# Optimization experiments

Hardware: AMD Instinct MI355X
Metric: run time of the kernel (lower is better)

## Reference

```python
import jax, jax.numpy as jnp
import numpy as np

TAU = 1.0
TOP_P = 0.9
EPS = 1e-5


def _nucleus_adj(X, W1, W2, W3):
    h = jnp.tanh(X @ W1.T)            # [N, d_attn]
    q = h @ W2.T                      # [N, d_attn]
    k = X @ W3.T                      # [N, d_attn]
    scores = (q @ k.T) / TAU          # [N, N]
    probs = jax.nn.softmax(scores, axis=-1)
    # nucleus (top-p): keep smallest prefix of desc-sorted probs covering mass p
    order = jnp.argsort(-probs, axis=-1)
    sp = jnp.take_along_axis(probs, order, axis=-1)
    cs = jnp.cumsum(sp, axis=-1)
    keep_sorted = (cs - sp) < TOP_P   # keep tokens before mass exceeds p (incl. crossing one)
    inv = jnp.argsort(order, axis=-1)
    keep = jnp.take_along_axis(keep_sorted, inv, axis=-1)
    A = jnp.where(keep, probs, 0.0)
    return A / jnp.sum(A, axis=-1, keepdims=True)


def _sequence_priors(N, dtype):
    # forward/backward chain priors (S=None case): row-stochastic shift matrices
    Rf = jnp.eye(N, k=-1, dtype=dtype).at[0, 0].set(1.0)
    Rb = jnp.eye(N, k=1, dtype=dtype).at[N - 1, N - 1].set(1.0)
    return Rf, Rb


def setup_inputs() -> dict:
    key = jax.random.key(0)
    ks = jax.random.split(key, 8)
    N, d_in, d_attn, steps = 4096, 512, 64, 2
    s = 0.02
    return {
        "X": jax.random.normal(ks[0], (N, d_in), jnp.float32),
        "W1": jax.random.normal(ks[1], (d_attn, d_in), jnp.float32) * s,
        "W2": jax.random.normal(ks[2], (d_attn, d_attn), jnp.float32) * s,
        "W3": jax.random.normal(ks[3], (d_attn, d_in), jnp.float32) * s,
        "U1": jax.random.normal(ks[4], (steps, d_in, d_in), jnp.float32) * s,
        "U2": jax.random.normal(ks[5], (steps, d_in, d_in), jnp.float32) * s,
        "U3": jax.random.normal(ks[6], (steps, d_in, d_in), jnp.float32) * s,
        "gamma": jnp.ones((d_in,), jnp.float32),
        "beta": jnp.zeros((d_in,), jnp.float32),
    }


def reference(X, W1, W2, W3, U1, U2, U3, gamma, beta):
    N = X.shape[0]
    steps = U1.shape[0]
    Rf, Rb = _sequence_priors(N, X.dtype)
    Z = jnp.zeros_like(X)
    Xf, Xb, Xa = X, X, X
    for n in range(steps):
        A = _nucleus_adj(Xa, W1, W2, W3)
        Xf = Rf @ Xf
        Xb = Rb @ Xb
        Xa = A @ Xa
        P = Xf @ U1[n].T + Xb @ U2[n].T
        F = Xa @ U3[n].T
        Z = Z + (P + F)  # dropout is identity in eval mode
    y = X + Z
    mu = jnp.mean(y, axis=-1, keepdims=True)
    var = jnp.var(y, axis=-1, keepdims=True)
    return (y - mu) * jax.lax.rsqrt(var + EPS) * gamma + beta
```

## Files before the change

kernel.cpp:

```cpp
#include <hip/hip_runtime.h>
#include <hip/hip_bf16.h>
#include <math.h>

typedef short bf16x8 __attribute__((ext_vector_type(8)));
typedef float f32x4 __attribute__((ext_vector_type(4)));
typedef unsigned short u16;

#define N_TOK  4096
#define D_IN   512
#define D_ATTN 64
#define NBI    1024
#define CAPW   128
#define TOPP   0.9f
#define LN_EPS 1e-5f
#define AMAXV  (N_TOK - 1)
#define FLTMAX 3.402823466e38f
#define MSCALE 524288.0f

__device__ __forceinline__ u16 f2bf(float f) {
  unsigned int u = __float_as_uint(f);
  return (u16)((u + 0x7FFFu + ((u >> 16) & 1u)) >> 16);
}

__device__ __forceinline__ unsigned mfix(float e) {
  return (unsigned)(e * MSCALE + 0.5f);
}

__device__ __forceinline__ void gload16(const u16* g, u16* l) {
  __builtin_amdgcn_global_load_lds(
      (const __attribute__((address_space(1))) unsigned int*)g,
      (__attribute__((address_space(3))) unsigned int*)l, 16, 0, 0);
}

template<int EPI, int NSEG, int KSEG, int BN>
__global__ __launch_bounds__(256)
void gemm128(const u16* __restrict__ A0, int lda0, int sh0, const u16* __restrict__ B0, int ldb0,
             const u16* __restrict__ A1, int lda1, int sh1, const u16* __restrict__ B1, int ldb1,
             const u16* __restrict__ A2, int lda2, int sh2, const u16* __restrict__ B2, int ldb2,
             float* __restrict__ Cf, u16* __restrict__ Cb, u16* __restrict__ CbT,
             int ldc, int ldct)
{
  constexpr int NF = BN / 32;
  __shared__ u16 sA[2][128 * 64];
  __shared__ u16 sB[2][BN * 64];

  const int tid  = threadIdx.x;
  const int wave = tid >> 6;
  const int lane = tid & 63;
  const int l15  = lane & 15;
  const int l4   = lane >> 4;
  const int brow = blockIdx.y << 7;
  const int bcol = blockIdx.x * BN;
  const int kz   = blockIdx.z * KSEG;
  const int wr64 = (wave >> 1) << 6;
  const int wcol = (wave & 1) * (BN >> 1);

  constexpr int IPSEG = KSEG >> 6;
  constexpr int TOTAL = NSEG * IPSEG;

  auto stage = [&](int buf, int it) {
    int seg = (NSEG == 1) ? 0 : (it / IPSEG);
    int kk  = (NSEG == 1) ? (it << 6) : ((it % IPSEG) << 6);
    const u16 *Ab, *Bb; int la, lb, sh;
    if (seg == 0)      { Ab = A0; la = lda0; sh = sh0; Bb = B0; lb = ldb0; }
    else if (seg == 1) { Ab = A1; la = lda1; sh = sh1; Bb = B1; lb = ldb1; }
    else               { Ab = A2; la = lda2; sh = sh2; Bb = B2; lb = ldb2; }
    kk += kz;
#pragma unroll
    for (int q = 0; q < 4; ++q) {
      int idx = q * 256 + tid;
      int row = idx >> 3;
      int chunk = (idx & 7) ^ (row & 7);
      int r = brow + row + sh;
      r = (r < 0) ? 0 : ((r > AMAXV) ? AMAXV : r);
      gload16(Ab + (size_t)r * la + kk + chunk * 8, &sA[buf][idx * 8]);
    }
#pragma unroll
    for (int q = 0; q < BN / 32; ++q) {
      int idx = q * 256 + tid;
      int row = idx >> 3;
      int chunk = (idx & 7) ^ (row & 7);
      gload16(Bb + (size_t)(bcol + row) * lb + kk + chunk * 8, &sB[buf][idx * 8]);
    }
  };

  f32x4 acc[4][NF];
#pragma unroll
  for (int m = 0; m < 4; ++m)
#pragma unroll
    for (int n = 0; n < NF; ++n) {
      acc[m][n][0] = 0.f; acc[m][n][1] = 0.f; acc[m][n][2] = 0.f; acc[m][n][3] = 0.f;
    }

  stage(0, 0);
  asm volatile("s_waitcnt vmcnt(0)" ::: "memory");
  __builtin_amdgcn_s_barrier();

  for (int i = 0; i < TOTAL; ++i) {
    const int c = i & 1;
    if (i + 1 < TOTAL) stage(c ^ 1, i + 1);
#pragma unroll
    for (int ks = 0; ks < 2; ++ks) {
      bf16x8 af[4], bfr[NF];
#pragma unroll
      for (int m = 0; m < 4; ++m) {
        int ar = wr64 + m * 16 + l15;
        af[m] = *(const bf16x8*)&sA[c][ar * 64 + (((ks << 2) + l4) ^ (ar & 7)) * 8];
      }
#pragma unroll
      for (int n = 0; n < NF; ++n) {
        int br = wcol + n * 16 + l15;
        bfr[n] = *(const bf16x8*)&sB[c][br * 64 + (((ks << 2) + l4) ^ (br & 7)) * 8];
      }
#pragma unroll
      for (int m = 0; m < 4; ++m)
#pragma unroll
        for (int n = 0; n < NF; ++n)
          acc[m][n] = __builtin_amdgcn_mfma_f32_16x16x32_bf16(af[m], bfr[n], acc[m][n], 0, 0, 0);
    }
    asm volatile("s_waitcnt vmcnt(0)" ::: "memory");
    __builtin_amdgcn_s_barrier();
  }

  float* Cf6 = (EPI == 6 && blockIdx.z) ? (float*)CbT : Cf;
#pragma unroll
  for (int m = 0; m < 4; ++m)
#pragma unroll
    for (int n = 0; n < NF; ++n)
#pragma unroll
      for (int r = 0; r < 4; ++r) {
        const int row = brow + wr64 + m * 16 + l4 * 4 + r;
        const int col = bcol + wcol + n * 16 + l15;
        const float v = acc[m][n][r];
        if (EPI == 0) Cf[(size_t)row * ldc + col] = v;
        if (EPI == 1) Cb[(size_t)row * ldc + col] = f2bf(tanhf(v));
        if (EPI == 2) Cb[(size_t)row * ldc + col] = f2bf(v);
        if (EPI == 3) Cf[(size_t)row * ldc + col] += v;
        if (EPI == 4) {
          u16 hv = f2bf(v);
          Cb [(size_t)row * ldc  + col] = hv;
          CbT[(size_t)col * ldct + row] = hv;
        }
        if (EPI == 5) {
          if (col < 64) Cb [(size_t)row * 64 + col]        = f2bf(tanhf(v));
          else          CbT[(size_t)row * 64 + (col - 64)] = f2bf(v);
        }
        if (EPI == 6) Cf6[(size_t)row * ldc + col] = v;
      }
}

__global__ __launch_bounds__(256)
void pvfix(const float* __restrict__ Zp0, const float* __restrict__ Zp1,
           u16* __restrict__ Xa, u16* __restrict__ XaT)
{
  __shared__ u16 tile[64][65];
  const int bx = blockIdx.x, by = blockIdx.y;
  const int t = threadIdx.x;
  const int tx = t & 15, ty = t >> 4;
#pragma unroll
  for (int i = 0; i < 4; ++i) {
    int r = by * 64 + ty + 16 * i;
    int c = bx * 64 + tx * 4;
    float4 a = *(const float4*)&Zp0[(size_t)r * D_IN + c];
    float4 b = *(const float4*)&Zp1[(size_t)r * D_IN + c];
    u16 q0 = f2bf(a.x + b.x), q1 = f2bf(a.y + b.y);
    u16 q2 = f2bf(a.z + b.z), q3 = f2bf(a.w + b.w);
    *(ushort4*)&Xa[(size_t)r * D_IN + c] = make_ushort4(q0, q1, q2, q3);
    tile[ty + 16 * i][tx * 4 + 0] = q0;
    tile[ty + 16 * i][tx * 4 + 1] = q1;
    tile[ty + 16 * i][tx * 4 + 2] = q2;
    tile[ty + 16 * i][tx * 4 + 3] = q3;
  }
  __syncthreads();
#pragma unroll
  for (int i = 0; i < 4; ++i) {
    int cc = ty + 16 * i;
    int rq = tx * 4;
    u16 o0 = tile[rq + 0][cc], o1 = tile[rq + 1][cc];
    u16 o2 = tile[rq + 2][cc], o3 = tile[rq + 3][cc];
    *(ushort4*)&XaT[(size_t)(bx * 64 + cc) * N_TOK + by * 64 + rq] =
        make_ushort4(o0, o1, o2, o3);
  }
}

__global__ __launch_bounds__(256)
void nucleus_block(const float* __restrict__ S, u16* __restrict__ A, int apitch)
{
  const int t = threadIdx.x;
  const int wv = t >> 6, ln = t & 63;

  __shared__ unsigned hist[4][NBI];
  __shared__ float ge[CAPW];
  __shared__ int   gcol[CAPW];
  __shared__ unsigned gm[CAPW];
  __shared__ unsigned char kf[CAPW];
  __shared__ float sMin[4], sMax[4], sDen[4];
  __shared__ int   sCnt[4], sS[4];
  __shared__ unsigned sScan[4];
  __shared__ unsigned s_Ab;
  __shared__ int   s_cnt;

  for (int rr = 0; rr < 2; ++rr) {
    const int row = blockIdx.x + rr * (N_TOK / 2);
    const float* srow = S + (size_t)row * N_TOK;
    u16* arow = A + (size_t)row * apitch;

    __syncthreads();

    float evf[16];
    float lmax = -FLTMAX, lmin = FLTMAX;
#pragma unroll
    for (int q = 0; q < 4; ++q) {
      float4 v = ((const float4*)srow)[q * 256 + t];
      evf[4*q+0] = v.x; evf[4*q+1] = v.y; evf[4*q+2] = v.z; evf[4*q+3] = v.w;
      lmax = fmaxf(lmax, fmaxf(fmaxf(v.x, v.y), fmaxf(v.z, v.w)));
      lmin = fminf(lmin, fminf(fminf(v.x, v.y), fminf(v.z, v.w)));
    }
#pragma unroll
    for (int o = 32; o; o >>= 1) {
      lmax = fmaxf(lmax, __shfl_xor(lmax, o));
      lmin = fminf(lmin, __shfl_xor(lmin, o));
    }
    if (ln == 0) { sMax[wv] = lmax; sMin[wv] = lmin; }
    __syncthreads();
    const float smax = fmaxf(fmaxf(sMax[0], sMax[1]), fmaxf(sMax[2], sMax[3]));
    const float smin = fminf(fminf(sMin[0], sMin[1]), fminf(sMin[2], sMin[3]));

#pragma unroll
    for (int j = 0; j < 16; ++j) evf[j] = __expf(evf[j] - smax);

    unsigned keepM = 0, cand = 0xFFFFu;
    unsigned Agt = 0, T = 0;
    bool haveT = false;
    float lo = __expf(smin - smax);
    float width = fmaxf(1.0f - lo, 1e-30f);

    for (int lev = 0; lev < 12; ++lev) {
      __syncthreads();
      {
        uint4 z; z.x = 0; z.y = 0; z.z = 0; z.w = 0;
        ((uint4*)hist[0])[t] = z; ((uint4*)hist[1])[t] = z;
        ((uint4*)hist[2])[t] = z; ((uint4*)hist[3])[t] = z;
      }
      int myCnt = __popc(cand);
      float cmin = FLTMAX, cmax = -FLTMAX;
#pragma unroll
      for (int j = 0; j < 16; ++j)
        if ((cand >> j) & 1) { float e = evf[j]; cmin = fminf(cmin, e); cmax = fmaxf(cmax, e); }
      int ct = myCnt;
#pragma unroll
      for (int o = 32; o; o >>= 1) {
        ct   += __shfl_xor(ct, o);
        cmin  = fminf(cmin, __shfl_xor(cmin, o));
        cmax  = fmaxf(cmax, __shfl_xor(cmax, o));
      }
      if (ln == 0) { sCnt[wv] = ct; sMin[wv] = cmin; sMax[wv] = cmax; }
      __syncthreads();
      const int tot = sCnt[0] + sCnt[1] + sCnt[2] + sCnt[3];
      cmin = fminf(fminf(sMin[0], sMin[1]), fminf(sMin[2], sMin[3]));
      cmax = fmaxf(fmaxf(sMax[0], sMax[1]), fmaxf(sMax[2], sMax[3]));

      if (tot == 0) break;

      if (haveT && (cmin == cmax || lev == 11)) {
        const float v = cmax;
        const unsigned mv = mfix(v);
        int r;
        if (T <= Agt) r = 0;
        else if (mv == 0) r = tot;
        else { unsigned need = T - Agt; r = (int)((need + mv - 1) / mv); if (r > tot) r = tot; }
        int cq[4], excl[4];
#pragma unroll
        for (int q = 0; q < 4; ++q) {
          cq[q] = __popc((cand >> (4 * q)) & 0xF);
          int sc = cq[q];
#pragma unroll
          for (int o = 1; o < 64; o <<= 1) { int u = __shfl_up(sc, o); if (ln >= o) sc += u; }
          excl[q] = sc - cq[q];
          if (ln == 63) hist[wv][NBI - 4 + q] = (unsigned)(excl[q] + cq[q]);
        }
        __syncthreads();
        int qtot[4], woffq[4];
#pragma unroll
        for (int q = 0; q < 4; ++q) {
          unsigned w0 = hist[0][NBI - 4 + q], w1 = hist[1][NBI - 4 + q],
                   w2 = hist[2][NBI - 4 + q], w3 = hist[3][NBI - 4 + q];
          woffq[q] = (wv > 0 ? (int)w0 : 0) + (wv > 1 ? (int)w1 : 0) + (wv > 2 ? (int)w2 : 0);
          qtot[q]  = (int)(w0 + w1 + w2 + w3);
        }
        int qbase = 0;
#pragma unroll
        for (int q = 0; q < 4; ++q) {
          int seen = 0;
#pragma unroll
          for (int jj = 0; jj < 4; ++jj) {
            int j = 4 * q + jj;
            if ((cand >> j) & 1) {
              int rank = qbase + woffq[q] + excl[q] + seen;
              if (rank < r) keepM |= 1u << j;
              ++seen;
            }
          }
          qbase += qtot[q];
        }
        break;
      }

      if (haveT && tot <= CAPW) {
        if (t == 0) s_cnt = 0;
        __syncthreads();
#pragma unroll
        for (int j = 0; j < 16; ++j) {
          if ((cand >> j) & 1) {
            int i = atomicAdd(&s_cnt, 1);
            ge[i] = evf[j];
            gm[i] = mfix(evf[j]);
            gcol[i] = ((j >> 2) << 10) + (t << 2) + (j & 3);
          }
        }
        __syncthreads();
        const int cnt = s_cnt;
        if (t < cnt) {
          float ei = ge[t]; int ci = gcol[t];
          unsigned m = Agt;
          for (int u = 0; u < cnt; ++u) {
            float el = ge[u];
            if (el > ei || (el == ei && gcol[u] < ci)) m += gm[u];
          }
          kf[t] = (m < T) ? 1 : 0;
        }
        __syncthreads();
        for (int u = 0; u < cnt; ++u) {
          int c = gcol[u];
          if (((c >> 2) & 255) == t && kf[u])
            keepM |= 1u << (((c >> 10) << 2) | (c & 3));
        }
        break;
      }

      const float scale = (float)NBI / width;
      __syncthreads();
      unsigned* Hw = hist[wv];
#pragma unroll
      for (int j = 0; j < 16; ++j) {
        if ((cand >> j) & 1) {
          float e = evf[j];
          int b = (int)((e - lo) * scale);
          b = (b < 0) ? 0 : ((b > NBI - 1) ? NBI - 1 : b);
          atomicAdd(&Hw[b], mfix(e));
        }
      }
      __syncthreads();
      unsigned hv[4];
      {
        uint4 a0 = ((const uint4*)hist[0])[t];
        uint4 a1 = ((const uint4*)hist[1])[t];
        uint4 a2 = ((const uint4*)hist[2])[t];
        uint4 a3 = ((const uint4*)hist[3])[t];
        hv[0] = a0.x + a1.x + a2.x + a3.x;
        hv[1] = a0.y + a1.y + a2.y + a3.y;
        hv[2] = a0.z + a1.z + a2.z + a3.z;
        hv[3] = a0.w + a1.w + a2.w + a3.w;
      }
      unsigned sl = (hv[0] + hv[1]) + (hv[2] + hv[3]);
      unsigned pv = sl;
#pragma unroll
      for (int o = 1; o < 64; o <<= 1) { unsigned u = __shfl_up(pv, o); if (ln >= o) pv += u; }
      if (ln == 63) sScan[wv] = pv;
      __syncthreads();
      const unsigned woff = (wv > 0 ? sScan[0] : 0u) + (wv > 1 ? sScan[1] : 0u) + (wv > 2 ? sScan[2] : 0u);
      const unsigned CM   = sScan[0] + sScan[1] + sScan[2] + sScan[3];
      if (!haveT) {
        T = (unsigned)((9ULL * (unsigned long long)CM) / 10ULL);
        haveT = true;
      }
      const unsigned incl = pv + woff;
      unsigned Arun = Agt + (CM - incl);
      int lb = -1; unsigned Ab = 0;
#pragma unroll
      for (int j = 3; j >= 0; --j) {
        unsigned bm = hv[j];
        if (Arun < T && Arun + bm >= T) { lb = j; Ab = Arun; }
        Arun += bm;
      }
      int bl = (lb >= 0) ? ((t << 2) | lb) : -1;
      int s = bl;
#pragma unroll
      for (int o = 32; o; o >>= 1) s = max(s, __shfl_xor(s, o));
      if (ln == 0) sS[wv] = s;
      __syncthreads();
      s = max(max(sS[0], sS[1]), max(sS[2], sS[3]));
      if (s < 0) { keepM |= cand; break; }
      if (bl == s) s_Ab = Ab;
      __syncthreads();
      const unsigned Abnd = s_Ab;
      unsigned nk = 0, nc = 0;
#pragma unroll
      for (int j = 0; j < 16; ++j) {
        if ((cand >> j) & 1) {
          float e = evf[j];
          int b = (int)((e - lo) * scale);
          b = (b < 0) ? 0 : ((b > NBI - 1) ? NBI - 1 : b);
          if (b > s) nk |= 1u << j;
          else if (b == s) nc |= 1u << j;
        }
      }
      keepM |= nk;
      cand = nc;
      Agt = Abnd;
      width = fmaxf(width * (1.0f / NBI), 1e-37f);
      lo = lo + (float)s * width;
    }

    float dl = 0.f;
#pragma unroll
    for (int j = 0; j < 16; ++j)
      if ((keepM >> j) & 1) dl += evf[j];
#pragma unroll
    for (int o = 32; o; o >>= 1) dl += __shfl_xor(dl, o);
    if (ln == 0) sDen[wv] = dl;
    __syncthreads();
    float den = sDen[0] + sDen[1] + sDen[2] + sDen[3];
    if (den <= 0.f) den = 1.f;
    const float invd = 1.0f / den;

#pragma unroll
    for (int q = 0; q < 4; ++q) {
      u16 rr4[4];
#pragma unroll
      for (int j = 0; j < 4; ++j) {
        int b = 4 * q + j;
        float val = ((keepM >> b) & 1) ? evf[b] * invd : 0.f;
        rr4[j] = f2bf(val);
      }
      ((ushort4*)arow)[q * 256 + t] = make_ushort4(rr4[0], rr4[1], rr4[2], rr4[3]);
    }
  }
}

__global__ void cvt_all(const float* __restrict__ X,  const float* __restrict__ W1,
                        const float* __restrict__ W3, const float* __restrict__ W2,
                        const float* __restrict__ U1, const float* __restrict__ U2,
                        const float* __restrict__ U3,
                        u16* __restrict__ Xbf, u16* __restrict__ Xa0,
                        u16* __restrict__ W13b, u16* __restrict__ W2b,
                        u16* __restrict__ U1b, u16* __restrict__ U2b, u16* __restrict__ U3b)
{
  const int NX = 524288, NW = 8192, NW2 = 1024, NU = 131072;
  const int TOT = NX + 2 * NW + NW2 + 3 * NU;
  const int stride = gridDim.x * 256;
  for (int i = blockIdx.x * 256 + threadIdx.x; i < TOT; i += stride) {
    const float* s; u16* d; int rel; bool dual = false;
    if (i < NX)                       { s = X;  d = Xbf;  rel = i; dual = true; }
    else if (i < NX + NW)             { s = W1; d = W13b; rel = i - NX; }
    else if (i < NX + 2*NW)           { s = W3; d = W13b + (size_t)4*NW; rel = i - NX - NW; }
    else if (i < NX + 2*NW + NW2)     { s = W2; d = W2b;  rel = i - NX - 2*NW; }
    else if (i < NX + 2*NW + NW2 + NU){ s = U1; d = U1b;  rel = i - NX - 2*NW - NW2; }
    else if (i < NX + 2*NW + NW2+2*NU){ s = U2; d = U2b;  rel = i - NX - 2*NW - NW2 - NU; }
    else                              { s = U3; d = U3b;  rel = i - NX - 2*NW - NW2 - 2*NU; }
    float4 v = ((const float4*)s)[rel];
    ushort4 o;
    o.x = f2bf(v.x); o.y = f2bf(v.y); o.z = f2bf(v.z); o.w = f2bf(v.w);
    ((ushort4*)d)[rel] = o;
    if (dual) ((ushort4*)Xa0)[rel] = o;
  }
}

__global__ __launch_bounds__(256)
void tpose_bf(const float* __restrict__ X, u16* __restrict__ XT)
{
  __shared__ u16 tile[32][33];
  const int bc = blockIdx.x * 32;
  const int br = blockIdx.y * 32;
  const int tx = threadIdx.x & 31, ty = threadIdx.x >> 5;
#pragma unroll
  for (int i = 0; i < 32; i += 8)
    tile[ty + i][tx] = f2bf(X[(size_t)(br + ty + i) * D_IN + bc + tx]);
  __syncthreads();
#pragma unroll
  for (int i = 0; i < 32; i += 8)
    XT[(size_t)(bc + ty + i) * N_TOK + br + tx] = tile[tx][ty + i];
}

__global__ __launch_bounds__(256)
void ln_kernel(const float* __restrict__ X, float* Z,
               const float* __restrict__ gamma, const float* __restrict__ beta)
{
  const int tid = threadIdx.x;
  __shared__ float red[4];
  __shared__ float s_mu, s_var;
  for (int rr = 0; rr < 2; ++rr) {
    const int row = blockIdx.x + rr * (N_TOK / 2);
    const size_t base = (size_t)row * D_IN;
    __syncthreads();
    float y0 = X[base + tid] + Z[base + tid];
    float y1 = X[base + tid + 256] + Z[base + tid + 256];
    float s = y0 + y1;
    for (int o = 32; o; o >>= 1) s += __shfl_xor(s, o);
    if ((tid & 63) == 0) red[tid >> 6] = s;
    __syncthreads();
    if (tid == 0) s_mu = (red[0] + red[1] + red[2] + red[3]) * (1.f / D_IN);
    __syncthreads();
    const float mu = s_mu;
    float d0 = y0 - mu, d1 = y1 - mu;
    float v = d0 * d0 + d1 * d1;
    for (int o = 32; o; o >>= 1) v += __shfl_xor(v, o);
    if ((tid & 63) == 0) red[tid >> 6] = v;
    __syncthreads();
    if (tid == 0) s_var = (red[0] + red[1] + red[2] + red[3]) * (1.f / D_IN);
    __syncthreads();
    const float rs = rsqrtf(s_var + LN_EPS);
    Z[base + tid]       = d0 * rs * gamma[tid]       + beta[tid];
    Z[base + tid + 256] = d1 * rs * gamma[tid + 256] + beta[tid + 256];
  }
}

extern "C" void kernel_launch(void* const* d_in, const int* in_sizes, int n_in,
                              void* d_out, int out_size, void* d_ws, size_t ws_size,
                              hipStream_t stream)
{
  const float* X     = (const float*)d_in[0];
  const float* W1    = (const float*)d_in[1];
  const float* W2    = (const float*)d_in[2];
  const float* W3    = (const float*)d_in[3];
  const float* U1    = (const float*)d_in[4];
  const float* U2    = (const float*)d_in[5];
  const float* U3    = (const float*)d_in[6];
  const float* gamma = (const float*)d_in[7];
  const float* beta  = (const float*)d_in[8];

  char* w = (char*)d_ws;
  float* S    = (float*)w;            w += (size_t)N_TOK * N_TOK * 4;
  u16* Xbf    = (u16*)w;              w += (size_t)N_TOK * D_IN * 2;
  u16* Xa0    = (u16*)w;              w += (size_t)N_TOK * D_IN * 2;
  u16* Xa1    = (u16*)w;              w += (size_t)N_TOK * D_IN * 2;
  u16* XaT0   = (u16*)w;              w += (size_t)D_IN * N_TOK * 2;
  u16* XaT1   = (u16*)w;              w += (size_t)D_IN * N_TOK * 2;
  u16* hb     = (u16*)w;              w += (size_t)N_TOK * D_ATTN * 2;
  u16* qb     = (u16*)w;              w += (size_t)N_TOK * D_ATTN * 2;
  u16* kb     = (u16*)w;              w += (size_t)N_TOK * D_ATTN * 2;
  u16* W13b   = (u16*)w;              w += (size_t)2 * D_ATTN * D_IN * 2;
  u16* W2b    = (u16*)w;              w += (size_t)D_ATTN * D_ATTN * 2;
  u16* U1b    = (u16*)w;              w += (size_t)2 * D_IN * D_IN * 2;
  u16* U2b    = (u16*)w;              w += (size_t)2 * D_IN * D_IN * 2;
  u16* U3b    = (u16*)w;              w += (size_t)2 * D_IN * D_IN * 2;

  size_t used = (size_t)(w - (char*)d_ws);
  u16* Abuf;
  int  apitch;
  if (ws_size >= used + (size_t)N_TOK * N_TOK * 2) {
    Abuf = (u16*)w;
    apitch = N_TOK;
    w += (size_t)N_TOK * N_TOK * 2;
  } else {
    Abuf = (u16*)S;
    apitch = 2 * N_TOK;
  }
  used = (size_t)(w - (char*)d_ws);
  float* Zp0 = nullptr;
  float* Zp1 = nullptr;
  const bool splitK = (ws_size >= used + 2 * (size_t)N_TOK * D_IN * 4);
  if (splitK) {
    Zp0 = (float*)w; w += (size_t)N_TOK * D_IN * 4;
    Zp1 = (float*)w; w += (size_t)N_TOK * D_IN * 4;
  }

  float* Z = (float*)d_out;

  hipMemsetAsync(d_out, 0, (size_t)N_TOK * D_IN * 4, stream);

  cvt_all<<<1024, 256, 0, stream>>>(X, W1, W3, W2, U1, U2, U3,
                                    Xbf, Xa0, W13b, W2b, U1b, U2b, U3b);
  tpose_bf<<<dim3(D_IN / 32, N_TOK / 32), 256, 0, stream>>>(X, XaT0);

  u16* XaC[2]  = {Xa0, Xa1};
  u16* XaTC[2] = {XaT0, XaT1};

  for (int n = 0; n < 2; ++n) {
    const int cur = n & 1, nxt = cur ^ 1;
    const size_t uoff = (size_t)n * D_IN * D_IN;
    gemm128<5, 1, D_IN, 64><<<dim3(2, 32), 256, 0, stream>>>(
        XaC[cur], D_IN, 0, W13b, D_IN,
        nullptr, 0, 0, nullptr, 0, nullptr, 0, 0, nullptr, 0,
        nullptr, hb, kb, 64, 64);
    gemm128<2, 1, D_ATTN, 64><<<dim3(1, 32), 256, 0, stream>>>(
        hb, D_ATTN, 0, W2b, D_ATTN,
        nullptr, 0, 0, nullptr, 0, nullptr, 0, 0, nullptr, 0,
        nullptr, qb, nullptr, D_ATTN, 0);
    gemm128<0, 1, D_ATTN, 128><<<dim3(32, 32), 256, 0, stream>>>(
        qb, D_ATTN, 0, kb, D_ATTN,
        nullptr, 0, 0, nullptr, 0, nullptr, 0, 0, nullptr, 0,
        S, nullptr, nullptr, N_TOK, 0);
    nucleus_block<<<N_TOK / 2, 256, 0, stream>>>(S, Abuf, apitch);
    if (splitK) {
      gemm128<6, 1, N_TOK / 2, 64><<<dim3(8, 32, 2), 256, 0, stream>>>(
          Abuf, apitch, 0, XaTC[cur], N_TOK,
          nullptr, 0, 0, nullptr, 0, nullptr, 0, 0, nullptr, 0,
          Zp0, nullptr, (u16*)Zp1, D_IN, 0);
      pvfix<<<dim3(D_IN / 64, N_TOK / 64), 256, 0, stream>>>(
          Zp0, Zp1, XaC[nxt], XaTC[nxt]);
    } else {
      gemm128<4, 1, N_TOK, 128><<<dim3(4, 32), 256, 0, stream>>>(
          Abuf, apitch, 0, XaTC[cur], N_TOK,
          nullptr, 0, 0, nullptr, 0, nullptr, 0, 0, nullptr, 0,
          nullptr, XaC[nxt], XaTC[nxt], D_IN, N_TOK);
    }
    gemm128<3, 3, D_IN, 64><<<dim3(8, 32), 256, 0, stream>>>(
        Xbf, D_IN, -(n + 1), U1b + uoff, D_IN,
        Xbf, D_IN,  (n + 1), U2b + uoff, D_IN,
        XaC[nxt], D_IN, 0,   U3b + uoff, D_IN,
        Z, nullptr, nullptr, D_IN, 0);
  }

  ln_kernel<<<N_TOK / 2, 256, 0, stream>>>(X, Z, gamma, beta);
}
```

Baseline: 367.7 us.

## Store scores as bf16 and compute nucleus denominator from fixed-point masses

The QK^T score matrix is now written as bf16 instead of fp32, which halves the write and read traffic of the 4096x4096 score buffer between the GEMM and the nucleus kernel. The nucleus kernel no longer computes a row minimum; the histogram starts on [0,1]. The final normalisation denominator comes from the accumulated fixed-point mass instead of a separate reduction pass, and the boundary-bin search is folded into a single packed 64-bit max reduction. Rounding scores to bf16 can change which tokens fall inside the top-p set, and the fixed-point denominator is slightly less exact.

```diff
diff --git a/kernel.cpp b/kernel.cpp
--- a/kernel.cpp
+++ b/kernel.cpp
@@ -5,6 +5,7 @@
 typedef short bf16x8 __attribute__((ext_vector_type(8)));
 typedef float f32x4 __attribute__((ext_vector_type(4)));
 typedef unsigned short u16;
+typedef unsigned long long u64;
 
 #define N_TOK  4096
 #define D_IN   512
@@ -20,6 +21,10 @@
 __device__ __forceinline__ u16 f2bf(float f) {
   unsigned int u = __float_as_uint(f);
   return (u16)((u + 0x7FFFu + ((u >> 16) & 1u)) >> 16);
+}
+
+__device__ __forceinline__ float bf2f(u16 v) {
+  return __uint_as_float(((unsigned)v) << 16);
 }
 
 __device__ __forceinline__ unsigned mfix(float e) {
@@ -184,47 +189,43 @@
 }
 
 __global__ __launch_bounds__(256)
-void nucleus_block(const float* __restrict__ S, u16* __restrict__ A, int apitch)
+void nucleus_block(const u16* __restrict__ S, u16* __restrict__ A, int apitch)
 {
   const int t = threadIdx.x;
   const int wv = t >> 6, ln = t & 63;
 
   __shared__ unsigned hist[4][NBI];
   __shared__ float ge[CAPW];
+  __shared__ unsigned gm[CAPW];
   __shared__ int   gcol[CAPW];
-  __shared__ unsigned gm[CAPW];
   __shared__ unsigned char kf[CAPW];
-  __shared__ float sMin[4], sMax[4], sDen[4];
-  __shared__ int   sCnt[4], sS[4];
+  __shared__ float sMax[4], sMin[4];
+  __shared__ int   sCnt[4];
   __shared__ unsigned sScan[4];
-  __shared__ unsigned s_Ab;
+  __shared__ u64   sKey[4];
   __shared__ int   s_cnt;
 
   for (int rr = 0; rr < 2; ++rr) {
     const int row = blockIdx.x + rr * (N_TOK / 2);
-    const float* srow = S + (size_t)row * N_TOK;
+    const u16* srow = S + (size_t)row * N_TOK;
     u16* arow = A + (size_t)row * apitch;
 
     __syncthreads();
 
     float evf[16];
-    float lmax = -FLTMAX, lmin = FLTMAX;
+    float lmax = -FLTMAX;
 #pragma unroll
     for (int q = 0; q < 4; ++q) {
-      float4 v = ((const float4*)srow)[q * 256 + t];
-      evf[4*q+0] = v.x; evf[4*q+1] = v.y; evf[4*q+2] = v.z; evf[4*q+3] = v.w;
-      lmax = fmaxf(lmax, fmaxf(fmaxf(v.x, v.y), fmaxf(v.z, v.w)));
-      lmin = fminf(lmin, fminf(fminf(v.x, v.y), fminf(v.z, v.w)));
-    }
-#pragma unroll
-    for (int o = 32; o; o >>= 1) {
-      lmax = fmaxf(lmax, __shfl_xor(lmax, o));
-      lmin = fminf(lmin, __shfl_xor(lmin, o));
-    }
-    if (ln == 0) { sMax[wv] = lmax; sMin[wv] = lmin; }
+      ushort4 v = ((const ushort4*)srow)[q * 256 + t];
+      float e0 = bf2f(v.x), e1 = bf2f(v.y), e2 = bf2f(v.z), e3 = bf2f(v.w);
+      evf[4*q+0] = e0; evf[4*q+1] = e1; evf[4*q+2] = e2; evf[4*q+3] = e3;
+      lmax = fmaxf(lmax, fmaxf(fmaxf(e0, e1), fmaxf(e2, e3)));
+    }
+#pragma unroll
+    for (int o = 32; o; o >>= 1) lmax = fmaxf(lmax, __shfl_xor(lmax, o));
+    if (ln == 0) sMax[wv] = lmax;
     __syncthreads();
     const float smax = fmaxf(fmaxf(sMax[0], sMax[1]), fmaxf(sMax[2], sMax[3]));
-    const float smin = fminf(fminf(sMin[0], sMin[1]), fminf(sMin[2], sMin[3]));
 
 #pragma unroll
     for (int j = 0; j < 16; ++j) evf[j] = __expf(evf[j] - smax);
@@ -232,113 +233,120 @@
     unsigned keepM = 0, cand = 0xFFFFu;
     unsigned Agt = 0, T = 0;
     bool haveT = false;
-    float lo = __expf(smin - smax);
-    float width = fmaxf(1.0f - lo, 1e-30f);
+    float lo = 0.f, width = 1.f;
+    u64 denInt = 0;
 
     for (int lev = 0; lev < 12; ++lev) {
-      __syncthreads();
+      if (lev > 0) {
+        int myCnt = __popc(cand);
+        float cmin = FLTMAX, cmax = -FLTMAX;
+#pragma unroll
+        for (int j = 0; j < 16; ++j)
+          if ((cand >> j) & 1) { float e = evf[j]; cmin = fminf(cmin, e); cmax = fmaxf(cmax, e); }
+        int ct = myCnt;
+#pragma unroll
+        for (int o = 32; o; o >>= 1) {
+          ct   += __shfl_xor(ct, o);
+          cmin  = fminf(cmin, __shfl_xor(cmin, o));
+          cmax  = fmaxf(cmax, __shfl_xor(cmax, o));
+        }
+        if (ln == 0) { sCnt[wv] = ct; sMin[wv] = cmin; sMax[wv] = cmax; }
+        __syncthreads();
+        const int tot = sCnt[0] + sCnt[1] + sCnt[2] + sCnt[3];
+        cmin = fminf(fminf(sMin[0], sMin[1]), fminf(sMin[2], sMin[3]));
+        cmax = fmaxf(fmaxf(sMax[0], sMax[1]), fmaxf(sMax[2], sMax[3]));
+
+        if (tot == 0) { denInt = Agt; break; }
+
+        if (cmin == cmax || lev == 11) {
+          const float v = cmax;
+          const unsigned mv = mfix(v);
+          int r;
+          if (T <= Agt) r = 0;
+          else if (mv == 0) r = tot;
+          else { unsigned need = T - Agt; r = (int)((need + mv - 1) / mv); if (r > tot) r = tot; }
+          int cq[4], excl[4];
+#pragma unroll
+          for (int q = 0; q < 4; ++q) {
+            cq[q] = __popc((cand >> (4 * q)) & 0xF);
+            int sc = cq[q];
+#pragma unroll
+            for (int o = 1; o < 64; o <<= 1) { int u = __shfl_up(sc, o); if (ln >= o) sc += u; }
+            excl[q] = sc - cq[q];
+            if (ln == 63) hist[wv][NBI - 4 + q] = (unsigned)(excl[q] + cq[q]);
+          }
+          __syncthreads();
+          int qtot[4], woffq[4];
+#pragma unroll
+          for (int q = 0; q < 4; ++q) {
+            unsigned w0 = hist[0][NBI - 4 + q], w1 = hist[1][NBI - 4 + q],
+                     w2 = hist[2][NBI - 4 + q], w3 = hist[3][NBI - 4 + q];
+            woffq[q] = (wv > 0 ? (int)w0 : 0) + (wv > 1 ? (int)w1 : 0) + (wv > 2 ? (int)w2 : 0);
+            qtot[q]  = (int)(w0 + w1 + w2 + w3);
+          }
+          int qbase = 0;
+#pragma unroll
+          for (int q = 0; q < 4; ++q) {
+            int seen = 0;
+#pragma unroll
+            for (int jj = 0; jj < 4; ++jj) {
+              int j = 4 * q + jj;
+              if ((cand >> j) & 1) {
+                int rank = qbase + woffq[q] + excl[q] + seen;
+                if (rank < r) keepM |= 1u << j;
+                ++seen;
+              }
+            }
+            qbase += qtot[q];
+          }
+          denInt = (u64)Agt + (u64)r * mv;
+          break;
+        }
+
+        if (tot <= CAPW) {
+          if (t == 0) s_cnt = 0;
+          __syncthreads();
+#pragma unroll
+          for (int j = 0; j < 16; ++j) {
+            if ((cand >> j) & 1) {
+              int i = atomicAdd(&s_cnt, 1);
+              ge[i] = evf[j];
+              gm[i] = mfix(evf[j]);
+              gcol[i] = ((j >> 2) << 10) + (t << 2) + (j & 3);
+            }
+          }
+          __syncthreads();
+          const int cnt = s_cnt;
+          if (t < cnt) {
+            float ei = ge[t]; int ci = gcol[t];
+            unsigned m = Agt;
+            for (int u = 0; u < cnt; ++u) {
+              float el = ge[u];
+              if (el > ei || (el == ei && gcol[u] < ci)) m += gm[u];
+            }
+            kf[t] = (m < T) ? 1 : 0;
+          }
+          __syncthreads();
+          u64 ks = 0;
+          for (int u = 0; u < cnt; ++u) {
+            if (kf[u]) {
+              ks += gm[u];
+              int c = gcol[u];
+              if (((c >> 2) & 255) == t)
+                keepM |= 1u << (((c >> 10) << 2) | (c & 3));
+            }
+          }
+          denInt = (u64)Agt + ks;
+          break;
+        }
+      }
+
+      const float scale = (float)NBI / width;
       {
         uint4 z; z.x = 0; z.y = 0; z.z = 0; z.w = 0;
         ((uint4*)hist[0])[t] = z; ((uint4*)hist[1])[t] = z;
         ((uint4*)hist[2])[t] = z; ((uint4*)hist[3])[t] = z;
       }
-      int myCnt = __popc(cand);
-      float cmin = FLTMAX, cmax = -FLTMAX;
-#pragma unroll
-      for (int j = 0; j < 16; ++j)
-        if ((cand >> j) & 1) { float e = evf[j]; cmin = fminf(cmin, e); cmax = fmaxf(cmax, e); }
-      int ct = myCnt;
-#pragma unroll
-      for (int o = 32; o; o >>= 1) {
-        ct   += __shfl_xor(ct, o);
-        cmin  = fminf(cmin, __shfl_xor(cmin, o));
-        cmax  = fmaxf(cmax, __shfl_xor(cmax, o));
-      }
-      if (ln == 0) { sCnt[wv] = ct; sMin[wv] = cmin; sMax[wv] = cmax; }
-      __syncthreads();
-      const int tot = sCnt[0] + sCnt[1] + sCnt[2] + sCnt[3];
-      cmin = fminf(fminf(sMin[0], sMin[1]), fminf(sMin[2], sMin[3]));
-      cmax = fmaxf(fmaxf(sMax[0], sMax[1]), fmaxf(sMax[2], sMax[3]));
-
-      if (tot == 0) break;
-
-      if (haveT && (cmin == cmax || lev == 11)) {
-        const float v = cmax;
-        const unsigned mv = mfix(v);
-        int r;
-        if (T <= Agt) r = 0;
-        else if (mv == 0) r = tot;
-        else { unsigned need = T - Agt; r = (int)((need + mv - 1) / mv); if (r > tot) r = tot; }
-        int cq[4], excl[4];
-#pragma unroll
-        for (int q = 0; q < 4; ++q) {
-          cq[q] = __popc((cand >> (4 * q)) & 0xF);
-          int sc = cq[q];
-#pragma unroll
-          for (int o = 1; o < 64; o <<= 1) { int u = __shfl_up(sc, o); if (ln >= o) sc += u; }
-          excl[q] = sc - cq[q];
-          if (ln == 63) hist[wv][NBI - 4 + q] = (unsigned)(excl[q] + cq[q]);
-        }
-        __syncthreads();
-        int qtot[4], woffq[4];
-#pragma unroll
-        for (int q = 0; q < 4; ++q) {
-          unsigned w0 = hist[0][NBI - 4 + q], w1 = hist[1][NBI - 4 + q],
-                   w2 = hist[2][NBI - 4 + q], w3 = hist[3][NBI - 4 + q];
-          woffq[q] = (wv > 0 ? (int)w0 : 0) + (wv > 1 ? (int)w1 : 0) + (wv > 2 ? (int)w2 : 0);
-          qtot[q]  = (int)(w0 + w1 + w2 + w3);
-        }
-        int qbase = 0;
-#pragma unroll
-        for (int q = 0; q < 4; ++q) {
-          int seen = 0;
-#pragma unroll
-          for (int jj = 0; jj < 4; ++jj) {
-            int j = 4 * q + jj;
-            if ((cand >> j) & 1) {
-              int rank = qbase + woffq[q] + excl[q] + seen;
-              if (rank < r) keepM |= 1u << j;
-              ++seen;
-            }
-          }
-          qbase += qtot[q];
-        }
-        break;
-      }
-
-      if (haveT && tot <= CAPW) {
-        if (t == 0) s_cnt = 0;
-        __syncthreads();
-#pragma unroll
-        for (int j = 0; j < 16; ++j) {
-          if ((cand >> j) & 1) {
-            int i = atomicAdd(&s_cnt, 1);
-            ge[i] = evf[j];
-            gm[i] = mfix(evf[j]);
-            gcol[i] = ((j >> 2) << 10) + (t << 2) + (j & 3);
-          }
-        }
-        __syncthreads();
-        const int cnt = s_cnt;
-        if (t < cnt) {
-          float ei = ge[t]; int ci = gcol[t];
-          unsigned m = Agt;
-          for (int u = 0; u < cnt; ++u) {
-            float el = ge[u];
-            if (el > ei || (el == ei && gcol[u] < ci)) m += gm[u];
-          }
-          kf[t] = (m < T) ? 1 : 0;
-        }
-        __syncthreads();
-        for (int u = 0; u < cnt; ++u) {
-          int c = gcol[u];
-          if (((c >> 2) & 255) == t && kf[u])
-            keepM |= 1u << (((c >> 10) << 2) | (c & 3));
-        }
-        break;
-      }
-
-      const float scale = (float)NBI / width;
       __syncthreads();
       unsigned* Hw = hist[wv];
 #pragma unroll
@@ -383,17 +391,18 @@
         if (Arun < T && Arun + bm >= T) { lb = j; Ab = Arun; }
         Arun += bm;
       }
-      int bl = (lb >= 0) ? ((t << 2) | lb) : -1;
-      int s = bl;
-#pragma unroll
-      for (int o = 32; o; o >>= 1) s = max(s, __shfl_xor(s, o));
-      if (ln == 0) sS[wv] = s;
+      u64 key = (lb >= 0) ? (((u64)(unsigned)(((t << 2) | lb) + 1) << 32) | (u64)Ab) : 0ULL;
+#pragma unroll
+      for (int o = 32; o; o >>= 1) { u64 k2 = __shfl_xor(key, o); if (k2 > key) key = k2; }
+      if (ln == 0) sKey[wv] = key;
       __syncthreads();
-      s = max(max(sS[0], sS[1]), max(sS[2], sS[3]));
-      if (s < 0) { keepM |= cand; break; }
-      if (bl == s) s_Ab = Ab;
-      __syncthreads();
-      const unsigned Abnd = s_Ab;
+      u64 kmax = sKey[0];
+      if (sKey[1] > kmax) kmax = sKey[1];
+      if (sKey[2] > kmax) kmax = sKey[2];
+      if (sKey[3] > kmax) kmax = sKey[3];
+      const int s = (int)(unsigned)(kmax >> 32) - 1;
+      if (s < 0) { keepM |= cand; denInt = (u64)Agt + CM; break; }
+      const unsigned Abnd = (unsigned)kmax;
       unsigned nk = 0, nc = 0;
 #pragma unroll
       for (int j = 0; j < 16; ++j) {
@@ -412,16 +421,8 @@
       lo = lo + (float)s * width;
     }
 
-    float dl = 0.f;
-#pragma unroll
-    for (int j = 0; j < 16; ++j)
-      if ((keepM >> j) & 1) dl += evf[j];
-#pragma unroll
-    for (int o = 32; o; o >>= 1) dl += __shfl_xor(dl, o);
-    if (ln == 0) sDen[wv] = dl;
-    __syncthreads();
-    float den = sDen[0] + sDen[1] + sDen[2] + sDen[3];
-    if (den <= 0.f) den = 1.f;
+    float den = (float)denInt * (1.0f / MSCALE);
+    if (denInt == 0) den = 1.f;
     const float invd = 1.0f / den;
 
 #pragma unroll
@@ -530,7 +531,7 @@
   const float* beta  = (const float*)d_in[8];
 
   char* w = (char*)d_ws;
-  float* S    = (float*)w;            w += (size_t)N_TOK * N_TOK * 4;
+  u16* S16    = (u16*)w;              w += (size_t)N_TOK * N_TOK * 2;
   u16* Xbf    = (u16*)w;              w += (size_t)N_TOK * D_IN * 2;
   u16* Xa0    = (u16*)w;              w += (size_t)N_TOK * D_IN * 2;
   u16* Xa1    = (u16*)w;              w += (size_t)N_TOK * D_IN * 2;
@@ -547,14 +548,12 @@
 
   size_t used = (size_t)(w - (char*)d_ws);
   u16* Abuf;
-  int  apitch;
+  int  apitch = N_TOK;
   if (ws_size >= used + (size_t)N_TOK * N_TOK * 2) {
     Abuf = (u16*)w;
-    apitch = N_TOK;
     w += (size_t)N_TOK * N_TOK * 2;
   } else {
-    Abuf = (u16*)S;
-    apitch = 2 * N_TOK;
+    Abuf = S16;
   }
   used = (size_t)(w - (char*)d_ws);
   float* Zp0 = nullptr;
@@ -587,11 +586,11 @@
         hb, D_ATTN, 0, W2b, D_ATTN,
         nullptr, 0, 0, nullptr, 0, nullptr, 0, 0, nullptr, 0,
         nullptr, qb, nullptr, D_ATTN, 0);
-    gemm128<0, 1, D_ATTN, 128><<<dim3(32, 32), 256, 0, stream>>>(
+    gemm128<2, 1, D_ATTN, 128><<<dim3(32, 32), 256, 0, stream>>>(
         qb, D_ATTN, 0, kb, D_ATTN,
         nullptr, 0, 0, nullptr, 0, nullptr, 0, 0, nullptr, 0,
-        S, nullptr, nullptr, N_TOK, 0);
-    nucleus_block<<<N_TOK / 2, 256, 0, stream>>>(S, Abuf, apitch);
+        nullptr, S16, nullptr, N_TOK, 0);
+    nucleus_block<<<N_TOK / 2, 256, 0, stream>>>(S16, Abuf, apitch);
     if (splitK) {
       gemm128<6, 1, N_TOK / 2, 64><<<dim3(8, 32, 2), 256, 0, stream>>>(
           Abuf, apitch, 0, XaTC[cur], N_TOK,
```

Measured after the change: 426.2 us. 1.16x slower.
